# Performance work log

Measured on AMD Instinct MI355X. Metric: run time of the kernel, lower is better.

Reference implementation:

```python
import jax, jax.numpy as jnp
import numpy as np

HEADS = 8
EPS = 1e-5


def _layernorm(x, g, b):
    mu = jnp.mean(x, axis=-1, keepdims=True)
    var = jnp.mean(jnp.square(x - mu), axis=-1, keepdims=True)
    return (x - mu) * jax.lax.rsqrt(var + EPS) * g + b


def setup_inputs() -> dict:
    key = jax.random.key(0)
    ks = jax.random.split(key, 10)
    B, S, D = 4, 2048, 256
    d_ff = 2 * D
    s = 0.02
    return {
        "x": jax.random.normal(ks[0], (B, S, D), dtype=jnp.float32),
        "ln1_g": jnp.ones((D,), jnp.float32),
        "ln1_b": jnp.zeros((D,), jnp.float32),
        "w_qkv": jax.random.normal(ks[1], (3 * D, D), jnp.float32) * s,
        "b_qkv": jnp.zeros((3 * D,), jnp.float32),
        "w_proj": jax.random.normal(ks[2], (D, D), jnp.float32) * s,
        "b_proj": jnp.zeros((D,), jnp.float32),
        "ln2_g": jnp.ones((D,), jnp.float32),
        "ln2_b": jnp.zeros((D,), jnp.float32),
        "w1": jax.random.normal(ks[3], (d_ff, D), jnp.float32) * s,
        "b1": jnp.zeros((d_ff,), jnp.float32),
        "w2": jax.random.normal(ks[4], (D, d_ff), jnp.float32) * s,
        "b2": jnp.zeros((D,), jnp.float32),
    }


def reference(x, ln1_g, ln1_b, w_qkv, b_qkv, w_proj, b_proj,
              ln2_g, ln2_b, w1, b1, w2, b2):
    B, S, D = x.shape
    H = HEADS
    dh = D // H
    scale = dh ** -0.5

    # --- attention sublayer (pre-LN) ---
    y = _layernorm(x, ln1_g, ln1_b)
    qkv = y @ w_qkv.T + b_qkv                       # [B,S,3D]
    qkv = qkv.reshape(B, S, 3, H, dh)
    q = jnp.transpose(qkv[:, :, 0], (0, 2, 1, 3))   # [B,H,S,dh]
    k = jnp.transpose(qkv[:, :, 1], (0, 2, 1, 3))
    v = jnp.transpose(qkv[:, :, 2], (0, 2, 1, 3))
    attn = jax.nn.softmax(jnp.einsum('bhsd,bhtd->bhst', q, k) * scale, axis=-1)
    ctx = jnp.einsum('bhst,bhtd->bhsd', attn, v)    # [B,H,S,dh]
    ctx = jnp.transpose(ctx, (0, 2, 1, 3)).reshape(B, S, D)
    x = x + ctx @ w_proj.T + b_proj

    # --- FFN sublayer (pre-LN) ---
    y = _layernorm(x, ln2_g, ln2_b)
    h = jax.nn.silu(y @ w1.T + b1)                  # [B,S,2D]
    x = x + h @ w2.T + b2
    return x
```

## Files before the change

### kernel.cpp

```cpp
#include <hip/hip_runtime.h>
#include <cstddef>

constexpr int kB   = 4;
constexpr int kS   = 2048;
constexpr int kD   = 256;
constexpr int kH   = 8;
constexpr int kDH  = 32;
constexpr int kDFF = 512;
constexpr int kM   = kB * kS;
constexpr float kEps = 1e-5f;
constexpr float kScaleL2E = 0.17677669529663687f * 1.4426950408889634f;

typedef float f32x4  __attribute__((ext_vector_type(4)));
typedef short bf16x8 __attribute__((ext_vector_type(8)));
typedef unsigned short u16;
typedef unsigned int   u32;

__device__ inline u16 f2bf(float x) {
    union { float f; unsigned u; } c; c.f = x;
    const unsigned r = c.u + 0x7fffu + ((c.u >> 16) & 1u);
    return (u16)(r >> 16);
}

__device__ inline u32 pk_trunc(float lo, float hi) {
    union { float f; u32 u; } a, b; a.f = lo; b.f = hi;
    return __builtin_amdgcn_perm(b.u, a.u, 0x07060302u);
}

__global__ __launch_bounds__(256)
void cast_w(const float* __restrict__ wqkv, const float* __restrict__ wproj,
            const float* __restrict__ w1, const float* __restrict__ w2,
            u16* __restrict__ out)
{
    const int e = (blockIdx.x * 256 + threadIdx.x) * 4;
    const float* src; int loc;
    if (e < 196608)      { src = wqkv;  loc = e; }
    else if (e < 262144) { src = wproj; loc = e - 196608; }
    else if (e < 393216) { src = w1;    loc = e - 262144; }
    else                 { src = w2;    loc = e - 393216; }
    const float4 v = *(const float4*)&src[loc];
    *(ushort4*)&out[e] = make_ushort4(f2bf(v.x), f2bf(v.y), f2bf(v.z), f2bf(v.w));
}

__global__ __launch_bounds__(256)
void ln_kernel(const float* __restrict__ x, const float* __restrict__ g,
               const float* __restrict__ b, u16* __restrict__ y)
{
    const int wave = threadIdx.x >> 6;
    const int lane = threadIdx.x & 63;
    const int row  = blockIdx.x * 4 + wave;
    const float4 v = *(const float4*)&x[(size_t)row * kD + lane * 4];
    float s1 = (v.x + v.y) + (v.z + v.w);
    float s2 = (v.x * v.x + v.y * v.y) + (v.z * v.z + v.w * v.w);
    #pragma unroll
    for (int off = 1; off < 64; off <<= 1) {
        s1 += __shfl_xor(s1, off);
        s2 += __shfl_xor(s2, off);
    }
    const float mu  = s1 * (1.0f / kD);
    const float var = s2 * (1.0f / kD) - mu * mu;
    const float inv = rsqrtf(var + kEps);
    const float4 g4 = *(const float4*)&g[lane * 4];
    const float4 b4 = *(const float4*)&b[lane * 4];
    *(ushort4*)&y[(size_t)row * kD + lane * 4] = make_ushort4(
        f2bf((v.x - mu) * inv * g4.x + b4.x),
        f2bf((v.y - mu) * inv * g4.y + b4.y),
        f2bf((v.z - mu) * inv * g4.z + b4.z),
        f2bf((v.w - mu) * inv * g4.w + b4.w));
}

template<int NT, int OUTMODE, bool RES, int KTOT>
__global__ __launch_bounds__(256)
void gemm_bf16(const u16* __restrict__ A, const u16* __restrict__ W,
               const float* __restrict__ bias, const float* __restrict__ res,
               float* __restrict__ Cf, u16* __restrict__ Cb,
               u16* __restrict__ KbP, u16* __restrict__ VtP, int N)
{
    __shared__ u16 Bs[NT][KTOT + 4];
    const int tid  = threadIdx.x;
    const int wave = tid >> 6;
    const int lane = tid & 63;
    const int quad = lane >> 4;
    const int l16  = lane & 15;
    const int m0 = blockIdx.x * 64;
    const int n0 = blockIdx.y * NT;

    {
        constexpr int TPR = 256 / NT;
        constexpr int CH  = KTOT / TPR;
        const int srow = tid % NT;
        const int sci  = tid / NT;
        const u16* wsrc = &W[(size_t)(n0 + srow) * KTOT + sci * CH];
        u16* wdst = &Bs[srow][sci * CH];
        #pragma unroll
        for (int t = 0; t < CH / 8; ++t)
            *(bf16x8*)&wdst[t * 8] = *(const bf16x8*)&wsrc[t * 8];
    }
    __syncthreads();

    f32x4 acc[NT / 16];
    #pragma unroll
    for (int ni = 0; ni < NT / 16; ++ni) acc[ni] = {0.f, 0.f, 0.f, 0.f};

    const u16* arow = &A[(size_t)(m0 + wave * 16 + l16) * KTOT];
    #pragma unroll 4
    for (int k0 = 0; k0 < KTOT; k0 += 32) {
        const bf16x8 a = *(const bf16x8*)&arow[k0 + quad * 8];
        #pragma unroll
        for (int ni = 0; ni < NT / 16; ++ni) {
            const bf16x8 bf = *(const bf16x8*)&Bs[ni * 16 + l16][k0 + quad * 8];
            acc[ni] = __builtin_amdgcn_mfma_f32_16x16x32_bf16(a, bf, acc[ni], 0, 0, 0);
        }
    }

    float bias_v[NT / 16];
    #pragma unroll
    for (int ni = 0; ni < NT / 16; ++ni) bias_v[ni] = bias[n0 + ni * 16 + l16];

    #pragma unroll
    for (int ni = 0; ni < NT / 16; ++ni) {
        #pragma unroll
        for (int r = 0; r < 4; ++r) {
            const int m = m0 + wave * 16 + quad * 4 + r;
            float v = acc[ni][r] + bias_v[ni];
            if (OUTMODE == 0) {
                const int n = n0 + ni * 16 + l16;
                if (RES) v += res[(size_t)m * N + n];
                Cf[(size_t)m * N + n] = v;
            } else if (OUTMODE == 1) {
                const int n = n0 + ni * 16 + l16;
                v = v / (1.0f + __expf(-v));
                Cb[(size_t)m * N + n] = f2bf(v);
            } else {
                const int rgn = n0 >> 8;
                const int nl  = (n0 & 255) + ni * 16 + l16;
                const int hh  = nl >> 5, dh = nl & 31;
                const int bb  = m >> 11, s = m & (kS - 1);
                const int bh  = bb * kH + hh;
                if (rgn == 0)
                    Cb[((size_t)bh * kS + s) * kDH + dh] = f2bf(v * kScaleL2E);
                else if (rgn == 1)
                    KbP[((size_t)bh * kS + s) * kDH + dh] = f2bf(v);
                else {
                    const int sp = (s & ~63) | (((s & 15) << 2) | ((s >> 4) & 3));
                    VtP[(((size_t)bh * (kS / 8) + (sp >> 3)) * kDH + dh) * 8 + (sp & 7)] = f2bf(v);
                }
            }
        }
    }
}

constexpr int kPStrU = 72;

__global__ __launch_bounds__(256, 4)
void attn_kernel(const u16* __restrict__ Qb, const u16* __restrict__ Kb,
                 const u16* __restrict__ Vp, u16* __restrict__ ctx)
{
    __shared__ __align__(16) u16 pbuf[4][32 * kPStrU];
    const int tid  = threadIdx.x;
    const int wave = tid >> 6;
    const int lane = tid & 63;
    const int quad = lane >> 4;
    const int l16  = lane & 15;
    const int h = blockIdx.y;
    const int b = blockIdx.z;
    const int bh = b * kH + h;
    const int qsub = wave >> 1;
    const int half = wave & 1;
    const int q0 = blockIdx.x * 64 + qsub * 32;

    bf16x8 aq[2];
    aq[0] = *(const bf16x8*)&Qb[((size_t)bh * kS + q0 + l16) * kDH + quad * 8];
    aq[1] = *(const bf16x8*)&Qb[((size_t)bh * kS + q0 + 16 + l16) * kDH + quad * 8];

    const u16* Kbase = Kb + (size_t)bh * kS * kDH;
    const u16* Vbase = Vp + (size_t)bh * kS * kDH;
    u16* pw = pbuf[wave];

    f32x4 O[2][2] = {};
    f32x4 lp[2] = {};
    const f32x4 zz = {0.f, 0.f, 0.f, 0.f};

    const int kbeg = half * (kS / 2);
    #pragma unroll 1
    for (int kt = kbeg; kt < kbeg + kS / 2; kt += 64) {
        bf16x8 kf[4];
        #pragma unroll
        for (int kg = 0; kg < 4; ++kg)
            kf[kg] = *(const bf16x8*)
                &Kbase[(size_t)(kt + kg * 16 + l16) * kDH + quad * 8];
        bf16x8 vf[2][2];
        #pragma unroll
        for (int ks = 0; ks < 2; ++ks)
            #pragma unroll
            for (int nf = 0; nf < 2; ++nf)
                vf[ks][nf] = *(const bf16x8*)
                    &Vbase[(size_t)((((kt + ks * 32 + quad * 8) >> 3) * kDH
                                     + nf * 16 + l16) << 3)];

        #pragma unroll
        for (int qb = 0; qb < 2; ++qb) {
            f32x4 S[4];
            #pragma unroll
            for (int kg = 0; kg < 4; ++kg)
                S[kg] = __builtin_amdgcn_mfma_f32_16x16x32_bf16(aq[qb], kf[kg], zz, 0, 0, 0);
            #pragma unroll
            for (int r = 0; r < 4; ++r) {
                const float e0 = exp2f(S[0][r]);
                const float e1 = exp2f(S[1][r]);
                const float e2 = exp2f(S[2][r]);
                const float e3 = exp2f(S[3][r]);
                lp[qb][r] += (e0 + e1) + (e2 + e3);
                uint2 pk;
                pk.x = pk_trunc(e0, e1);
                pk.y = pk_trunc(e2, e3);
                *(uint2*)&pw[(qb * 16 + quad * 4 + r) * kPStrU + l16 * 4] = pk;
            }
        }

        #pragma unroll
        for (int qb = 0; qb < 2; ++qb)
            #pragma unroll
            for (int ks = 0; ks < 2; ++ks) {
                const bf16x8 pA = *(const bf16x8*)
                    &pw[(qb * 16 + l16) * kPStrU + ks * 32 + quad * 8];
                O[qb][0] = __builtin_amdgcn_mfma_f32_16x16x32_bf16(pA, vf[ks][0], O[qb][0], 0, 0, 0);
                O[qb][1] = __builtin_amdgcn_mfma_f32_16x16x32_bf16(pA, vf[ks][1], O[qb][1], 0, 0, 0);
            }
    }

    #pragma unroll
    for (int off = 1; off < 16; off <<= 1)
        #pragma unroll
        for (int qb = 0; qb < 2; ++qb)
            #pragma unroll
            for (int r = 0; r < 4; ++r)
                lp[qb][r] += __shfl_xor(lp[qb][r], off);

    __syncthreads();
    float* cb = (float*)&pbuf[0][0] + qsub * (32 * 33);
    if (half == 1) {
        #pragma unroll
        for (int qb = 0; qb < 2; ++qb)
            #pragma unroll
            for (int r = 0; r < 4; ++r) {
                const int row = qb * 16 + quad * 4 + r;
                cb[row * 33 + l16]      = O[qb][0][r];
                cb[row * 33 + 16 + l16] = O[qb][1][r];
                if (l16 == 0) cb[row * 33 + 32] = lp[qb][r];
            }
    }
    __syncthreads();
    if (half == 0) {
        #pragma unroll
        for (int qb = 0; qb < 2; ++qb)
            #pragma unroll
            for (int r = 0; r < 4; ++r) {
                const int row = qb * 16 + quad * 4 + r;
                const float l   = lp[qb][r] + cb[row * 33 + 32];
                const float inv = 1.0f / l;
                const float o0 = O[qb][0][r] + cb[row * 33 + l16];
                const float o1 = O[qb][1][r] + cb[row * 33 + 16 + l16];
                const int q = q0 + row;
                u16* crow = ctx + ((size_t)(b * kS + q)) * kD + h * kDH;
                crow[l16]      = f2bf(o0 * inv);
                crow[16 + l16] = f2bf(o1 * inv);
            }
    }
}

extern "C" void kernel_launch(void* const* d_in, const int* in_sizes, int n_in,
                              void* d_out, int out_size, void* d_ws, size_t ws_size,
                              hipStream_t stream)
{
    const float* x      = (const float*)d_in[0];
    const float* ln1_g  = (const float*)d_in[1];
    const float* ln1_b  = (const float*)d_in[2];
    const float* w_qkv  = (const float*)d_in[3];
    const float* b_qkv  = (const float*)d_in[4];
    const float* w_proj = (const float*)d_in[5];
    const float* b_proj = (const float*)d_in[6];
    const float* ln2_g  = (const float*)d_in[7];
    const float* ln2_b  = (const float*)d_in[8];
    const float* w1     = (const float*)d_in[9];
    const float* b1     = (const float*)d_in[10];
    const float* w2     = (const float*)d_in[11];
    const float* b2     = (const float*)d_in[12];
    float* out = (float*)d_out;

    char* ws = (char*)d_ws;
    u16* y   = (u16*)ws;
    u16* Qb  = (u16*)(ws + ((size_t)4  << 20));
    u16* Kb  = (u16*)(ws + ((size_t)8  << 20));
    u16* Vp  = (u16*)(ws + ((size_t)12 << 20));
    u16* ctx = (u16*)(ws + ((size_t)16 << 20));
    u16* h   = (u16*)(ws + ((size_t)4  << 20));
    u16* Wb  = (u16*)(ws + ((size_t)20 << 20));
    u16* wb_qkv  = Wb;
    u16* wb_proj = Wb + 196608;
    u16* wb1     = Wb + 262144;
    u16* wb2     = Wb + 393216;

    const dim3 blk(256);

    cast_w<<<dim3(512), blk, 0, stream>>>(w_qkv, w_proj, w1, w2, Wb);
    ln_kernel<<<dim3(kM / 4), blk, 0, stream>>>(x, ln1_g, ln1_b, y);
    gemm_bf16<64, 2, false, 256><<<dim3(kM / 64, 12), blk, 0, stream>>>(
        y, wb_qkv, b_qkv, nullptr, nullptr, Qb, Kb, Vp, 0);
    attn_kernel<<<dim3(kS / 64, kH, kB), blk, 0, stream>>>(Qb, Kb, Vp, ctx);
    gemm_bf16<32, 0, true, 256><<<dim3(kM / 64, kD / 32), blk, 0, stream>>>(
        ctx, wb_proj, b_proj, x, out, nullptr, nullptr, nullptr, kD);
    ln_kernel<<<dim3(kM / 4), blk, 0, stream>>>(out, ln2_g, ln2_b, y);
    gemm_bf16<64, 1, false, 256><<<dim3(kM / 64, kDFF / 64), blk, 0, stream>>>(
        y, wb1, b1, nullptr, nullptr, h, nullptr, nullptr, kDFF);
    gemm_bf16<32, 0, true, 512><<<dim3(kM / 64, kD / 32), blk, 0, stream>>>(
        h, wb2, b2, out, out, nullptr, nullptr, nullptr, kD);
}
```

Before: 192.2 us.

## Fuse layernorm and weight bf16 cast into GEMM prologues

Removes the separate weight-cast kernel and both layernorm kernels. Each GEMM block now converts its fp32 weight tile to bf16 while loading it into shared memory. The LN-fed GEMMs normalize their 64 input rows on the fly into a shared-memory A tile. This cuts three launches and the round trips of the bf16 y and weight buffers, at the cost of redundant LN and cast work in every column-block (12 or 8 per row tile) and more shared memory per block.

```diff
diff --git a/kernel.cpp b/kernel.cpp
--- a/kernel.cpp
+++ b/kernel.cpp
@@ -27,56 +27,18 @@
     return __builtin_amdgcn_perm(b.u, a.u, 0x07060302u);
 }
 
+template<int NT, int OUTMODE, bool RES, int KTOT, bool LNA>
 __global__ __launch_bounds__(256)
-void cast_w(const float* __restrict__ wqkv, const float* __restrict__ wproj,
-            const float* __restrict__ w1, const float* __restrict__ w2,
-            u16* __restrict__ out)
+void gemm_fused(const void* __restrict__ Ain, const float* __restrict__ Wf,
+                const float* __restrict__ bias,
+                const float* __restrict__ lng, const float* __restrict__ lnb,
+                const float* __restrict__ res,
+                float* __restrict__ Cf, u16* __restrict__ Cb,
+                u16* __restrict__ KbP, u16* __restrict__ VtP, int N)
 {
-    const int e = (blockIdx.x * 256 + threadIdx.x) * 4;
-    const float* src; int loc;
-    if (e < 196608)      { src = wqkv;  loc = e; }
-    else if (e < 262144) { src = wproj; loc = e - 196608; }
-    else if (e < 393216) { src = w1;    loc = e - 262144; }
-    else                 { src = w2;    loc = e - 393216; }
-    const float4 v = *(const float4*)&src[loc];
-    *(ushort4*)&out[e] = make_ushort4(f2bf(v.x), f2bf(v.y), f2bf(v.z), f2bf(v.w));
-}
-
-__global__ __launch_bounds__(256)
-void ln_kernel(const float* __restrict__ x, const float* __restrict__ g,
-               const float* __restrict__ b, u16* __restrict__ y)
-{
-    const int wave = threadIdx.x >> 6;
-    const int lane = threadIdx.x & 63;
-    const int row  = blockIdx.x * 4 + wave;
-    const float4 v = *(const float4*)&x[(size_t)row * kD + lane * 4];
-    float s1 = (v.x + v.y) + (v.z + v.w);
-    float s2 = (v.x * v.x + v.y * v.y) + (v.z * v.z + v.w * v.w);
-    #pragma unroll
-    for (int off = 1; off < 64; off <<= 1) {
-        s1 += __shfl_xor(s1, off);
-        s2 += __shfl_xor(s2, off);
-    }
-    const float mu  = s1 * (1.0f / kD);
-    const float var = s2 * (1.0f / kD) - mu * mu;
-    const float inv = rsqrtf(var + kEps);
-    const float4 g4 = *(const float4*)&g[lane * 4];
-    const float4 b4 = *(const float4*)&b[lane * 4];
-    *(ushort4*)&y[(size_t)row * kD + lane * 4] = make_ushort4(
-        f2bf((v.x - mu) * inv * g4.x + b4.x),
-        f2bf((v.y - mu) * inv * g4.y + b4.y),
-        f2bf((v.z - mu) * inv * g4.z + b4.z),
-        f2bf((v.w - mu) * inv * g4.w + b4.w));
-}
-
-template<int NT, int OUTMODE, bool RES, int KTOT>
-__global__ __launch_bounds__(256)
-void gemm_bf16(const u16* __restrict__ A, const u16* __restrict__ W,
-               const float* __restrict__ bias, const float* __restrict__ res,
-               float* __restrict__ Cf, u16* __restrict__ Cb,
-               u16* __restrict__ KbP, u16* __restrict__ VtP, int N)
-{
-    __shared__ u16 Bs[NT][KTOT + 4];
+    constexpr int BSTR = KTOT + 4;
+    __shared__ u16 Bs[NT * BSTR];
+    __shared__ u16 As[LNA ? 64 * 260 : 1];
     const int tid  = threadIdx.x;
     const int wave = tid >> 6;
     const int lane = tid & 63;
@@ -90,11 +52,40 @@
         constexpr int CH  = KTOT / TPR;
         const int srow = tid % NT;
         const int sci  = tid / NT;
-        const u16* wsrc = &W[(size_t)(n0 + srow) * KTOT + sci * CH];
-        u16* wdst = &Bs[srow][sci * CH];
-        #pragma unroll
-        for (int t = 0; t < CH / 8; ++t)
-            *(bf16x8*)&wdst[t * 8] = *(const bf16x8*)&wsrc[t * 8];
+        const float* wsrc = &Wf[(size_t)(n0 + srow) * KTOT + sci * CH];
+        u16* wdst = &Bs[srow * BSTR + sci * CH];
+        #pragma unroll
+        for (int t = 0; t < CH / 4; ++t) {
+            const float4 wv = *(const float4*)&wsrc[t * 4];
+            *(ushort4*)&wdst[t * 4] = make_ushort4(
+                f2bf(wv.x), f2bf(wv.y), f2bf(wv.z), f2bf(wv.w));
+        }
+    }
+
+    if constexpr (LNA) {
+        const float* Af = (const float*)Ain;
+        const float4 g4 = *(const float4*)&lng[lane * 4];
+        const float4 b4 = *(const float4*)&lnb[lane * 4];
+        #pragma unroll 4
+        for (int rr = 0; rr < 16; ++rr) {
+            const int row = m0 + wave * 16 + rr;
+            const float4 v = *(const float4*)&Af[(size_t)row * kD + lane * 4];
+            float s1 = (v.x + v.y) + (v.z + v.w);
+            float s2 = (v.x * v.x + v.y * v.y) + (v.z * v.z + v.w * v.w);
+            #pragma unroll
+            for (int off = 1; off < 64; off <<= 1) {
+                s1 += __shfl_xor(s1, off);
+                s2 += __shfl_xor(s2, off);
+            }
+            const float mu  = s1 * (1.0f / kD);
+            const float var = s2 * (1.0f / kD) - mu * mu;
+            const float inv = rsqrtf(var + kEps);
+            *(ushort4*)&As[(wave * 16 + rr) * 260 + lane * 4] = make_ushort4(
+                f2bf((v.x - mu) * inv * g4.x + b4.x),
+                f2bf((v.y - mu) * inv * g4.y + b4.y),
+                f2bf((v.z - mu) * inv * g4.z + b4.z),
+                f2bf((v.w - mu) * inv * g4.w + b4.w));
+        }
     }
     __syncthreads();
 
@@ -102,13 +93,17 @@
     #pragma unroll
     for (int ni = 0; ni < NT / 16; ++ni) acc[ni] = {0.f, 0.f, 0.f, 0.f};
 
-    const u16* arow = &A[(size_t)(m0 + wave * 16 + l16) * KTOT];
+    const u16* Ab = (const u16*)Ain;
     #pragma unroll 4
     for (int k0 = 0; k0 < KTOT; k0 += 32) {
-        const bf16x8 a = *(const bf16x8*)&arow[k0 + quad * 8];
+        bf16x8 a;
+        if constexpr (LNA)
+            a = *(const bf16x8*)&As[(wave * 16 + l16) * 260 + k0 + quad * 8];
+        else
+            a = *(const bf16x8*)&Ab[(size_t)(m0 + wave * 16 + l16) * KTOT + k0 + quad * 8];
         #pragma unroll
         for (int ni = 0; ni < NT / 16; ++ni) {
-            const bf16x8 bf = *(const bf16x8*)&Bs[ni * 16 + l16][k0 + quad * 8];
+            const bf16x8 bf = *(const bf16x8*)&Bs[(ni * 16 + l16) * BSTR + k0 + quad * 8];
             acc[ni] = __builtin_amdgcn_mfma_f32_16x16x32_bf16(a, bf, acc[ni], 0, 0, 0);
         }
     }
@@ -289,30 +284,25 @@
     float* out = (float*)d_out;
 
     char* ws = (char*)d_ws;
-    u16* y   = (u16*)ws;
-    u16* Qb  = (u16*)(ws + ((size_t)4  << 20));
-    u16* Kb  = (u16*)(ws + ((size_t)8  << 20));
-    u16* Vp  = (u16*)(ws + ((size_t)12 << 20));
-    u16* ctx = (u16*)(ws + ((size_t)16 << 20));
-    u16* h   = (u16*)(ws + ((size_t)4  << 20));
-    u16* Wb  = (u16*)(ws + ((size_t)20 << 20));
-    u16* wb_qkv  = Wb;
-    u16* wb_proj = Wb + 196608;
-    u16* wb1     = Wb + 262144;
-    u16* wb2     = Wb + 393216;
+    u16* Qb  = (u16*)ws;
+    u16* Kb  = (u16*)(ws + ((size_t)4  << 20));
+    u16* Vp  = (u16*)(ws + ((size_t)8  << 20));
+    u16* ctx = (u16*)(ws + ((size_t)12 << 20));
+    u16* h   = (u16*)ws;
 
     const dim3 blk(256);
 
-    cast_w<<<dim3(512), blk, 0, stream>>>(w_qkv, w_proj, w1, w2, Wb);
-    ln_kernel<<<dim3(kM / 4), blk, 0, stream>>>(x, ln1_g, ln1_b, y);
-    gemm_bf16<64, 2, false, 256><<<dim3(kM / 64, 12), blk, 0, stream>>>(
-        y, wb_qkv, b_qkv, nullptr, nullptr, Qb, Kb, Vp, 0);
+    gemm_fused<64, 2, false, 256, true><<<dim3(kM / 64, 12), blk, 0, stream>>>(
+        x, w_qkv, b_qkv, ln1_g, ln1_b, nullptr,
+        nullptr, Qb, Kb, Vp, 0);
     attn_kernel<<<dim3(kS / 64, kH, kB), blk, 0, stream>>>(Qb, Kb, Vp, ctx);
-    gemm_bf16<32, 0, true, 256><<<dim3(kM / 64, kD / 32), blk, 0, stream>>>(
-        ctx, wb_proj, b_proj, x, out, nullptr, nullptr, nullptr, kD);
-    ln_kernel<<<dim3(kM / 4), blk, 0, stream>>>(out, ln2_g, ln2_b, y);
-    gemm_bf16<64, 1, false, 256><<<dim3(kM / 64, kDFF / 64), blk, 0, stream>>>(
-        y, wb1, b1, nullptr, nullptr, h, nullptr, nullptr, kDFF);
-    gemm_bf16<32, 0, true, 512><<<dim3(kM / 64, kD / 32), blk, 0, stream>>>(
-        h, wb2, b2, out, out, nullptr, nullptr, nullptr, kD);
-}
+    gemm_fused<32, 0, true, 256, false><<<dim3(kM / 64, kD / 32), blk, 0, stream>>>(
+        ctx, w_proj, b_proj, nullptr, nullptr, x,
+        out, nullptr, nullptr, nullptr, kD);
+    gemm_fused<64, 1, false, 256, true><<<dim3(kM / 64, kDFF / 64), blk, 0, stream>>>(
+        out, w1, b1, ln2_g, ln2_b, nullptr,
+        nullptr, h, nullptr, nullptr, kDFF);
+    gemm_fused<32, 0, true, 512, false><<<dim3(kM / 64, kD / 32), blk, 0, stream>>>(
+        h, w2, b2, nullptr, nullptr, out,
+        out, nullptr, nullptr, nullptr, kD);
+}
```

Measured after the change: 214.7 us. 1.12x slower.

## Fuse weight bf16 cast into GEMM loads and widen attention key tile

Applied to the files above, without the earlier changes.

Drops the separate weight-cast kernel. Each GEMM block now reads fp32 weights and converts them to bf16 while filling shared memory, which removes a launch and a workspace round trip but repeats the conversion in every block that shares a weight tile. The attention kernel now handles 128 keys per iteration instead of 64, with a new V permuted layout matching 128-key tiles and a wider P staging buffer. It also drops the occupancy hint from launch_bounds, which raises register pressure and may reduce waves per CU.

```diff
diff --git a/kernel.cpp b/kernel.cpp
--- a/kernel.cpp
+++ b/kernel.cpp
@@ -25,21 +25,6 @@
 __device__ inline u32 pk_trunc(float lo, float hi) {
     union { float f; u32 u; } a, b; a.f = lo; b.f = hi;
     return __builtin_amdgcn_perm(b.u, a.u, 0x07060302u);
-}
-
-__global__ __launch_bounds__(256)
-void cast_w(const float* __restrict__ wqkv, const float* __restrict__ wproj,
-            const float* __restrict__ w1, const float* __restrict__ w2,
-            u16* __restrict__ out)
-{
-    const int e = (blockIdx.x * 256 + threadIdx.x) * 4;
-    const float* src; int loc;
-    if (e < 196608)      { src = wqkv;  loc = e; }
-    else if (e < 262144) { src = wproj; loc = e - 196608; }
-    else if (e < 393216) { src = w1;    loc = e - 262144; }
-    else                 { src = w2;    loc = e - 393216; }
-    const float4 v = *(const float4*)&src[loc];
-    *(ushort4*)&out[e] = make_ushort4(f2bf(v.x), f2bf(v.y), f2bf(v.z), f2bf(v.w));
 }
 
 __global__ __launch_bounds__(256)
@@ -71,12 +56,13 @@
 
 template<int NT, int OUTMODE, bool RES, int KTOT>
 __global__ __launch_bounds__(256)
-void gemm_bf16(const u16* __restrict__ A, const u16* __restrict__ W,
+void gemm_bf16(const u16* __restrict__ A, const float* __restrict__ Wf,
                const float* __restrict__ bias, const float* __restrict__ res,
                float* __restrict__ Cf, u16* __restrict__ Cb,
                u16* __restrict__ KbP, u16* __restrict__ VtP, int N)
 {
-    __shared__ u16 Bs[NT][KTOT + 4];
+    constexpr int BSTR = KTOT + 4;
+    __shared__ u16 Bs[NT * BSTR];
     const int tid  = threadIdx.x;
     const int wave = tid >> 6;
     const int lane = tid & 63;
@@ -86,15 +72,16 @@
     const int n0 = blockIdx.y * NT;
 
     {
-        constexpr int TPR = 256 / NT;
-        constexpr int CH  = KTOT / TPR;
-        const int srow = tid % NT;
-        const int sci  = tid / NT;
-        const u16* wsrc = &W[(size_t)(n0 + srow) * KTOT + sci * CH];
-        u16* wdst = &Bs[srow][sci * CH];
-        #pragma unroll
-        for (int t = 0; t < CH / 8; ++t)
-            *(bf16x8*)&wdst[t * 8] = *(const bf16x8*)&wsrc[t * 8];
+        constexpr int ITS = (NT * KTOT) / 1024;
+        #pragma unroll
+        for (int it = 0; it < ITS; ++it) {
+            const int e   = it * 1024 + tid * 4;
+            const int row = e / KTOT;
+            const int col = e & (KTOT - 1);
+            const float4 wv = *(const float4*)&Wf[(size_t)(n0 + row) * KTOT + col];
+            *(ushort4*)&Bs[row * BSTR + col] = make_ushort4(
+                f2bf(wv.x), f2bf(wv.y), f2bf(wv.z), f2bf(wv.w));
+        }
     }
     __syncthreads();
 
@@ -108,21 +95,18 @@
         const bf16x8 a = *(const bf16x8*)&arow[k0 + quad * 8];
         #pragma unroll
         for (int ni = 0; ni < NT / 16; ++ni) {
-            const bf16x8 bf = *(const bf16x8*)&Bs[ni * 16 + l16][k0 + quad * 8];
+            const bf16x8 bf = *(const bf16x8*)&Bs[(ni * 16 + l16) * BSTR + k0 + quad * 8];
             acc[ni] = __builtin_amdgcn_mfma_f32_16x16x32_bf16(a, bf, acc[ni], 0, 0, 0);
         }
     }
 
-    float bias_v[NT / 16];
-    #pragma unroll
-    for (int ni = 0; ni < NT / 16; ++ni) bias_v[ni] = bias[n0 + ni * 16 + l16];
-
     #pragma unroll
     for (int ni = 0; ni < NT / 16; ++ni) {
+        const float bias_v = bias[n0 + ni * 16 + l16];
         #pragma unroll
         for (int r = 0; r < 4; ++r) {
             const int m = m0 + wave * 16 + quad * 4 + r;
-            float v = acc[ni][r] + bias_v[ni];
+            float v = acc[ni][r] + bias_v;
             if (OUTMODE == 0) {
                 const int n = n0 + ni * 16 + l16;
                 if (RES) v += res[(size_t)m * N + n];
@@ -142,17 +126,19 @@
                 else if (rgn == 1)
                     KbP[((size_t)bh * kS + s) * kDH + dh] = f2bf(v);
                 else {
-                    const int sp = (s & ~63) | (((s & 15) << 2) | ((s >> 4) & 3));
-                    VtP[(((size_t)bh * (kS / 8) + (sp >> 3)) * kDH + dh) * 8 + (sp & 7)] = f2bf(v);
+                    const int so = s & 127;
+                    const int p  = ((so & 15) << 3) | (so >> 4);
+                    VtP[((size_t)bh * (kS / 128) + (s >> 7)) * 4096
+                        + (p >> 3) * 256 + dh * 8 + (p & 7)] = f2bf(v);
                 }
             }
         }
     }
 }
 
-constexpr int kPStrU = 72;
-
-__global__ __launch_bounds__(256, 4)
+constexpr int kPStrU = 136;
+
+__global__ __launch_bounds__(256)
 void attn_kernel(const u16* __restrict__ Qb, const u16* __restrict__ Kb,
                  const u16* __restrict__ Vp, u16* __restrict__ ctx)
 {
@@ -183,45 +169,54 @@
 
     const int kbeg = half * (kS / 2);
     #pragma unroll 1
-    for (int kt = kbeg; kt < kbeg + kS / 2; kt += 64) {
-        bf16x8 kf[4];
-        #pragma unroll
-        for (int kg = 0; kg < 4; ++kg)
+    for (int kt = kbeg; kt < kbeg + kS / 2; kt += 128) {
+        bf16x8 kf[8];
+        #pragma unroll
+        for (int kg = 0; kg < 8; ++kg)
             kf[kg] = *(const bf16x8*)
                 &Kbase[(size_t)(kt + kg * 16 + l16) * kDH + quad * 8];
-        bf16x8 vf[2][2];
+        const u16* vtile = Vbase + (size_t)(kt >> 7) * 4096;
+        bf16x8 vf[4][2];
         #pragma unroll
         for (int ks = 0; ks < 2; ++ks)
             #pragma unroll
             for (int nf = 0; nf < 2; ++nf)
                 vf[ks][nf] = *(const bf16x8*)
-                    &Vbase[(size_t)((((kt + ks * 32 + quad * 8) >> 3) * kDH
-                                     + nf * 16 + l16) << 3)];
+                    &vtile[(ks * 4 + quad) * 256 + (nf * 16 + l16) * 8];
 
         #pragma unroll
         for (int qb = 0; qb < 2; ++qb) {
-            f32x4 S[4];
-            #pragma unroll
-            for (int kg = 0; kg < 4; ++kg)
+            f32x4 S[8];
+            #pragma unroll
+            for (int kg = 0; kg < 8; ++kg)
                 S[kg] = __builtin_amdgcn_mfma_f32_16x16x32_bf16(aq[qb], kf[kg], zz, 0, 0, 0);
             #pragma unroll
             for (int r = 0; r < 4; ++r) {
-                const float e0 = exp2f(S[0][r]);
-                const float e1 = exp2f(S[1][r]);
-                const float e2 = exp2f(S[2][r]);
-                const float e3 = exp2f(S[3][r]);
-                lp[qb][r] += (e0 + e1) + (e2 + e3);
-                uint2 pk;
-                pk.x = pk_trunc(e0, e1);
-                pk.y = pk_trunc(e2, e3);
-                *(uint2*)&pw[(qb * 16 + quad * 4 + r) * kPStrU + l16 * 4] = pk;
+                float e[8];
+                #pragma unroll
+                for (int kg = 0; kg < 8; ++kg) e[kg] = exp2f(S[kg][r]);
+                lp[qb][r] += ((e[0] + e[1]) + (e[2] + e[3]))
+                           + ((e[4] + e[5]) + (e[6] + e[7]));
+                uint4 pk;
+                pk.x = pk_trunc(e[0], e[1]);
+                pk.y = pk_trunc(e[2], e[3]);
+                pk.z = pk_trunc(e[4], e[5]);
+                pk.w = pk_trunc(e[6], e[7]);
+                *(uint4*)&pw[(qb * 16 + quad * 4 + r) * kPStrU + l16 * 8] = pk;
             }
         }
 
         #pragma unroll
+        for (int ks = 2; ks < 4; ++ks)
+            #pragma unroll
+            for (int nf = 0; nf < 2; ++nf)
+                vf[ks][nf] = *(const bf16x8*)
+                    &vtile[(ks * 4 + quad) * 256 + (nf * 16 + l16) * 8];
+
+        #pragma unroll
         for (int qb = 0; qb < 2; ++qb)
             #pragma unroll
-            for (int ks = 0; ks < 2; ++ks) {
+            for (int ks = 0; ks < 4; ++ks) {
                 const bf16x8 pA = *(const bf16x8*)
                     &pw[(qb * 16 + l16) * kPStrU + ks * 32 + quad * 8];
                 O[qb][0] = __builtin_amdgcn_mfma_f32_16x16x32_bf16(pA, vf[ks][0], O[qb][0], 0, 0, 0);
@@ -289,30 +284,24 @@
     float* out = (float*)d_out;
 
     char* ws = (char*)d_ws;
-    u16* y   = (u16*)ws;
-    u16* Qb  = (u16*)(ws + ((size_t)4  << 20));
-    u16* Kb  = (u16*)(ws + ((size_t)8  << 20));
-    u16* Vp  = (u16*)(ws + ((size_t)12 << 20));
-    u16* ctx = (u16*)(ws + ((size_t)16 << 20));
-    u16* h   = (u16*)(ws + ((size_t)4  << 20));
-    u16* Wb  = (u16*)(ws + ((size_t)20 << 20));
-    u16* wb_qkv  = Wb;
-    u16* wb_proj = Wb + 196608;
-    u16* wb1     = Wb + 262144;
-    u16* wb2     = Wb + 393216;
+    u16* Qb  = (u16*)ws;
+    u16* Kb  = (u16*)(ws + ((size_t)4  << 20));
+    u16* Vp  = (u16*)(ws + ((size_t)8  << 20));
+    u16* ctx = (u16*)(ws + ((size_t)12 << 20));
+    u16* y   = (u16*)(ws + ((size_t)16 << 20));
+    u16* h   = (u16*)ws;
 
     const dim3 blk(256);
 
-    cast_w<<<dim3(512), blk, 0, stream>>>(w_qkv, w_proj, w1, w2, Wb);
     ln_kernel<<<dim3(kM / 4), blk, 0, stream>>>(x, ln1_g, ln1_b, y);
     gemm_bf16<64, 2, false, 256><<<dim3(kM / 64, 12), blk, 0, stream>>>(
-        y, wb_qkv, b_qkv, nullptr, nullptr, Qb, Kb, Vp, 0);
+        y, w_qkv, b_qkv, nullptr, nullptr, Qb, Kb, Vp, 0);
     attn_kernel<<<dim3(kS / 64, kH, kB), blk, 0, stream>>>(Qb, Kb, Vp, ctx);
     gemm_bf16<32, 0, true, 256><<<dim3(kM / 64, kD / 32), blk, 0, stream>>>(
-        ctx, wb_proj, b_proj, x, out, nullptr, nullptr, nullptr, kD);
+        ctx, w_proj, b_proj, x, out, nullptr, nullptr, nullptr, kD);
     ln_kernel<<<dim3(kM / 4), blk, 0, stream>>>(out, ln2_g, ln2_b, y);
     gemm_bf16<64, 1, false, 256><<<dim3(kM / 64, kDFF / 64), blk, 0, stream>>>(
-        y, wb1, b1, nullptr, nullptr, h, nullptr, nullptr, kDFF);
+        y, w1, b1, nullptr, nullptr, h, nullptr, nullptr, kDFF);
     gemm_bf16<32, 0, true, 512><<<dim3(kM / 64, kD / 32), blk, 0, stream>>>(
-        h, wb2, b2, out, out, nullptr, nullptr, nullptr, kD);
-}
+        h, w2, b2, out, out, nullptr, nullptr, nullptr, kD);
+}
```

Result: no change. 188.7 us (-1.9%).
